# Kernel tuning notes

Measured on AMD Instinct MI355X. Metric: run time of the kernel, lower is better.

Reference implementation:

```python
import jax, jax.numpy as jnp
import numpy as np

EPS = 1e-5

def _point_batch_norm(x, gamma, beta):
    # BatchNorm1d over channel dim of (B, N, C): stats over (B, N), biased var (training mode)
    mu = jnp.mean(x, axis=(0, 1))
    var = jnp.var(x, axis=(0, 1))
    return (x - mu) * jax.lax.rsqrt(var + EPS) * gamma + beta

def setup_inputs() -> dict:
    key = jax.random.key(0)
    ks = jax.random.split(key, 10)
    B, M, N, K = 4, 16384, 32768, 16
    C, Cs, O = 64, 64, 64
    curr_coords = jax.random.normal(ks[0], (B, M, 3), jnp.float32)
    curr_feat = jax.random.normal(ks[1], (B, M, C), jnp.float32)
    skip_coords = jax.random.normal(ks[2], (B, N, 3), jnp.float32)
    skip_feat = jax.random.normal(ks[3], (B, N, Cs), jnp.float32)
    upsampling_idxs = jax.random.randint(ks[4], (B, N, K), 0, M, jnp.int64)
    s1 = 1.0 / np.sqrt(C)
    s2 = 1.0 / np.sqrt(Cs)
    W1 = jax.random.uniform(ks[5], (C, O), jnp.float32, -s1, s1)
    b1 = jax.random.uniform(ks[6], (O,), jnp.float32, -s1, s1)
    W2 = jax.random.uniform(ks[7], (Cs, O), jnp.float32, -s2, s2)
    b2 = jax.random.uniform(ks[8], (O,), jnp.float32, -s2, s2)
    g1 = jnp.ones((O,), jnp.float32); beta1 = jnp.zeros((O,), jnp.float32)
    g2 = jnp.ones((O,), jnp.float32); beta2 = jnp.zeros((O,), jnp.float32)
    return {
        "curr_coords": curr_coords, "curr_feat": curr_feat,
        "skip_coords": skip_coords, "skip_feat": skip_feat,
        "upsampling_idxs": upsampling_idxs,
        "W1": W1, "b1": b1, "g1": g1, "beta1": beta1,
        "W2": W2, "b2": b2, "g2": g2, "beta2": beta2,
    }

def reference(curr_coords, curr_feat, skip_coords, skip_feat, upsampling_idxs,
              W1, b1, g1, beta1, W2, b2, g2, beta2):
    # Gather K-NN neighbor features per skip point: (B, N, K, C), then max over K
    gathered = jax.vmap(lambda f, i: f[i])(curr_feat, upsampling_idxs)
    pooled = jnp.max(gathered, axis=2)  # (B, N, C)
    # proj: Linear -> PointBatchNorm -> ReLU
    h = jax.nn.relu(_point_batch_norm(pooled @ W1 + b1, g1, beta1))
    # proj_skip on skip features
    hs = jax.nn.relu(_point_batch_norm(skip_feat @ W2 + b2, g2, beta2))
    return jnp.concatenate([skip_coords, h, hs], axis=-1)  # (B, N, 3 + 2*O)
```

## Files before the change

kernel.cpp:

```cpp
#include <hip/hip_runtime.h>
#include <hip/hip_bf16.h>

#define BB 4
#define MM 16384
#define NN 32768
#define KK 16
#define ROWS (BB * NN)
#define OUTW 131
#define RPW 32
#define A_BLOCKS (ROWS / (RPW * 4))

__global__ __launch_bounds__(256) void k_pool_proj(
    const float* __restrict__ cf, const int* __restrict__ idxs,
    const float* __restrict__ scoord,
    const float* __restrict__ W1, const float* __restrict__ b1,
    float* __restrict__ out, float* __restrict__ acc)
{
    __shared__ float pool[4][64];
    __shared__ float lsum[64], lsq[64];
    const int lane = threadIdx.x & 63;
    const int wv   = threadIdx.x >> 6;
    if (threadIdx.x < 64) { lsum[threadIdx.x] = 0.f; lsq[threadIdx.x] = 0.f; }
    __syncthreads();

    float w[64];
#pragma unroll
    for (int c = 0; c < 64; ++c) w[c] = W1[c * 64 + lane];
    const float bias = b1[lane];

    float psum = 0.f, psq = 0.f;
    const int gw = blockIdx.x * 4 + wv;
    for (int r0 = 0; r0 < RPW; ++r0) {
        const int r = gw * RPW + r0;
        const int b = r >> 15;
        int mi = 0;
        if (lane < KK) mi = idxs[r * KK + lane];
        float pmax = -3.402823466e38f;
#pragma unroll
        for (int k = 0; k < KK; ++k) {
            const int m = __shfl(mi, k);
            pmax = fmaxf(pmax, cf[(((b << 14) + m) << 6) + lane]);
        }
        pool[wv][lane] = pmax;
        __builtin_amdgcn_wave_barrier();

        float y = bias;
#pragma unroll
        for (int c = 0; c < 64; ++c) y = fmaf(pool[wv][c], w[c], y);
        __builtin_amdgcn_wave_barrier();

        const size_t ob = (size_t)r * OUTW;
        out[ob + 3 + lane] = y;
        if (lane < 3) out[ob + lane] = scoord[r * 3 + lane];
        psum += y; psq += y * y;
    }
    atomicAdd(&lsum[lane], psum);
    atomicAdd(&lsq[lane], psq);
    __syncthreads();
    if (threadIdx.x < 64) {
        atomicAdd(&acc[threadIdx.x],      lsum[threadIdx.x]);
        atomicAdd(&acc[64 + threadIdx.x], lsq[threadIdx.x]);
    }
}

__global__ __launch_bounds__(256) void k_skip_proj(
    const float* __restrict__ sf,
    const float* __restrict__ W2, const float* __restrict__ b2,
    float* __restrict__ out, float* __restrict__ acc)
{
    __shared__ float srow[4][64];
    __shared__ float lsum[64], lsq[64];
    const int lane = threadIdx.x & 63;
    const int wv   = threadIdx.x >> 6;
    if (threadIdx.x < 64) { lsum[threadIdx.x] = 0.f; lsq[threadIdx.x] = 0.f; }
    __syncthreads();

    float w[64];
#pragma unroll
    for (int c = 0; c < 64; ++c) w[c] = W2[c * 64 + lane];
    const float bias = b2[lane];

    float psum = 0.f, psq = 0.f;
    const int gw = blockIdx.x * 4 + wv;
    for (int r0 = 0; r0 < RPW; ++r0) {
        const int r = gw * RPW + r0;
        srow[wv][lane] = sf[(size_t)r * 64 + lane];
        __builtin_amdgcn_wave_barrier();

        float y = bias;
#pragma unroll
        for (int c = 0; c < 64; ++c) y = fmaf(srow[wv][c], w[c], y);
        __builtin_amdgcn_wave_barrier();

        const size_t ob = (size_t)r * OUTW;
        out[ob + 67 + lane] = y;
        psum += y; psq += y * y;
    }
    atomicAdd(&lsum[lane], psum);
    atomicAdd(&lsq[lane], psq);
    __syncthreads();
    if (threadIdx.x < 64) {
        atomicAdd(&acc[128 + threadIdx.x], lsum[threadIdx.x]);
        atomicAdd(&acc[192 + threadIdx.x], lsq[threadIdx.x]);
    }
}

__global__ void k_stats(float* __restrict__ ws,
                        const float* __restrict__ g1, const float* __restrict__ be1,
                        const float* __restrict__ g2, const float* __restrict__ be2)
{
    const int o = threadIdx.x;
    const float inv = 1.0f / (float)ROWS;
    float m1 = ws[o] * inv;
    float v1 = ws[64 + o] * inv - m1 * m1;
    float a1 = g1[o] * rsqrtf(v1 + 1e-5f);
    ws[256 + o] = a1;
    ws[384 + o] = be1[o] - m1 * a1;
    float m2 = ws[128 + o] * inv;
    float v2 = ws[192 + o] * inv - m2 * m2;
    float a2 = g2[o] * rsqrtf(v2 + 1e-5f);
    ws[256 + 64 + o] = a2;
    ws[384 + 64 + o] = be2[o] - m2 * a2;
}

__global__ __launch_bounds__(256) void k_finalize(float* __restrict__ out,
                                                  const float* __restrict__ ws)
{
    const size_t T  = (size_t)gridDim.x * blockDim.x;
    const size_t t0 = (size_t)blockIdx.x * blockDim.x + threadIdx.x;
#pragma unroll
    for (int i = 0; i < 4; ++i) {
        const size_t e = t0 + (size_t)i * T;
        const size_t r = e >> 7;
        const int    j = (int)(e & 127);
        const size_t ad = r * OUTW + 3 + j;
        const float v = out[ad];
        out[ad] = fmaxf(fmaf(v, ws[256 + j], ws[384 + j]), 0.f);
    }
}

extern "C" void kernel_launch(void* const* d_in, const int* in_sizes, int n_in,
                              void* d_out, int out_size, void* d_ws, size_t ws_size,
                              hipStream_t stream)
{
    const float* cf     = (const float*)d_in[1];
    const float* scoord = (const float*)d_in[2];
    const float* sf     = (const float*)d_in[3];
    const int*   idxs   = (const int*)  d_in[4];
    const float* W1     = (const float*)d_in[5];
    const float* b1     = (const float*)d_in[6];
    const float* g1     = (const float*)d_in[7];
    const float* be1    = (const float*)d_in[8];
    const float* W2     = (const float*)d_in[9];
    const float* b2     = (const float*)d_in[10];
    const float* g2     = (const float*)d_in[11];
    const float* be2    = (const float*)d_in[12];
    float* out = (float*)d_out;
    float* ws  = (float*)d_ws;

    hipMemsetAsync(ws, 0, 256 * sizeof(float), stream);
    k_pool_proj<<<A_BLOCKS, 256, 0, stream>>>(cf, idxs, scoord, W1, b1, out, ws);
    k_skip_proj<<<A_BLOCKS, 256, 0, stream>>>(sf, W2, b2, out, ws);
    k_stats<<<1, 64, 0, stream>>>(ws, g1, be1, g2, be2);
    k_finalize<<<16384, 256, 0, stream>>>(out, ws);
}
```

Baseline: 290.1 us.

## Fuse batch-norm finalize into projection kernels via grid barrier, keep rows in LDS

Each projection kernel now holds its pre-norm outputs in shared memory, accumulates channel statistics, waits at a software grid-wide barrier, then applies batch norm and ReLU and writes the final output once. This drops the separate stats and finalize kernels and their full read-modify-write pass over the output. It also maps pool blocks to XCDs by batch for L2 locality, uses readlane broadcasts instead of LDS for the matvec, and prefetches indices and skip rows. The spin barrier relies on all 1024 blocks being co-resident, which risks deadlock if occupancy is lower than assumed.

```diff
diff --git a/kernel.cpp b/kernel.cpp
--- a/kernel.cpp
+++ b/kernel.cpp
@@ -1,5 +1,4 @@
 #include <hip/hip_runtime.h>
-#include <hip/hip_bf16.h>
 
 #define BB 4
 #define MM 16384
@@ -8,134 +7,171 @@
 #define ROWS (BB * NN)
 #define OUTW 131
 #define RPW 32
-#define A_BLOCKS (ROWS / (RPW * 4))
-
-__global__ __launch_bounds__(256) void k_pool_proj(
+#define GRID_A 1024
+#define GRID_B 1024
+
+
+__device__ __forceinline__ float bcast(float v, int sl) {
+    return __int_as_float(__builtin_amdgcn_readlane(__float_as_int(v), sl));
+}
+
+__device__ __forceinline__ void grid_barrier(int* bar, int nblk) {
+    __threadfence();
+    __syncthreads();
+    if (threadIdx.x == 0) {
+        __hip_atomic_fetch_add(bar, 1, __ATOMIC_ACQ_REL, __HIP_MEMORY_SCOPE_AGENT);
+        while (__hip_atomic_load(bar, __ATOMIC_ACQUIRE, __HIP_MEMORY_SCOPE_AGENT) < nblk)
+            __builtin_amdgcn_s_sleep(8);
+    }
+    __syncthreads();
+}
+
+__global__ __launch_bounds__(256, 4) void k_pool_proj(
     const float* __restrict__ cf, const int* __restrict__ idxs,
     const float* __restrict__ scoord,
     const float* __restrict__ W1, const float* __restrict__ b1,
-    float* __restrict__ out, float* __restrict__ acc)
+    const float* __restrict__ g1, const float* __restrict__ be1,
+    float* __restrict__ out, float* __restrict__ ws)
 {
-    __shared__ float pool[4][64];
+    __shared__ float ysav[4][RPW][64];
     __shared__ float lsum[64], lsq[64];
     const int lane = threadIdx.x & 63;
     const int wv   = threadIdx.x >> 6;
     if (threadIdx.x < 64) { lsum[threadIdx.x] = 0.f; lsq[threadIdx.x] = 0.f; }
     __syncthreads();
 
-    float w[64];
-#pragma unroll
-    for (int c = 0; c < 64; ++c) w[c] = W1[c * 64 + lane];
+    const int w     = blockIdx.x;
+    const int xcd   = w & 7;
+    const int batch = xcd >> 1;
+    const int lb    = (w >> 3) + ((xcd & 1) << 7);
+    const int rbase = batch * NN + (lb * 4 + wv) * RPW;
+
+    float wr[64];
+#pragma unroll
+    for (int c = 0; c < 64; ++c) wr[c] = W1[c * 64 + lane];
     const float bias = b1[lane];
+    const float* cfb = cf + ((size_t)batch * MM * 64);
 
     float psum = 0.f, psq = 0.f;
-    const int gw = blockIdx.x * 4 + wv;
-    for (int r0 = 0; r0 < RPW; ++r0) {
-        const int r = gw * RPW + r0;
-        const int b = r >> 15;
-        int mi = 0;
-        if (lane < KK) mi = idxs[r * KK + lane];
-        float pmax = -3.402823466e38f;
-#pragma unroll
-        for (int k = 0; k < KK; ++k) {
-            const int m = __shfl(mi, k);
-            pmax = fmaxf(pmax, cf[(((b << 14) + m) << 6) + lane]);
+    int mi4 = idxs[(size_t)rbase * KK + lane];
+    for (int r0 = 0; r0 < RPW; r0 += 4) {
+        int mi4n = 0;
+        if (r0 + 4 < RPW) mi4n = idxs[(size_t)(rbase + r0 + 4) * KK + lane];
+#pragma unroll
+        for (int rr = 0; rr < 4; ++rr) {
+            float p0 = -3.402823466e38f, p1 = p0;
+#pragma unroll
+            for (int k = 0; k < KK; k += 2) {
+                const int m0 = __builtin_amdgcn_readlane(mi4, (rr << 4) + k);
+                const int m1 = __builtin_amdgcn_readlane(mi4, (rr << 4) + k + 1);
+                p0 = fmaxf(p0, cfb[((size_t)m0 << 6) + lane]);
+                p1 = fmaxf(p1, cfb[((size_t)m1 << 6) + lane]);
+            }
+            const float pmax = fmaxf(p0, p1);
+            float a0 = 0.f, a1 = 0.f, a2 = 0.f, a3 = 0.f;
+#pragma unroll
+            for (int c = 0; c < 64; c += 4) {
+                a0 = fmaf(bcast(pmax, c + 0), wr[c + 0], a0);
+                a1 = fmaf(bcast(pmax, c + 1), wr[c + 1], a1);
+                a2 = fmaf(bcast(pmax, c + 2), wr[c + 2], a2);
+                a3 = fmaf(bcast(pmax, c + 3), wr[c + 3], a3);
+            }
+            const float y = bias + ((a0 + a1) + (a2 + a3));
+            ysav[wv][r0 + rr][lane] = y;
+            psum += y; psq += y * y;
+            const int r = rbase + r0 + rr;
+            if (lane < 3) out[(size_t)r * OUTW + lane] = scoord[(size_t)r * 3 + lane];
         }
-        pool[wv][lane] = pmax;
-        __builtin_amdgcn_wave_barrier();
-
-        float y = bias;
-#pragma unroll
-        for (int c = 0; c < 64; ++c) y = fmaf(pool[wv][c], w[c], y);
-        __builtin_amdgcn_wave_barrier();
-
-        const size_t ob = (size_t)r * OUTW;
-        out[ob + 3 + lane] = y;
-        if (lane < 3) out[ob + lane] = scoord[r * 3 + lane];
-        psum += y; psq += y * y;
-    }
+        mi4 = mi4n;
+    }
+
     atomicAdd(&lsum[lane], psum);
     atomicAdd(&lsq[lane], psq);
     __syncthreads();
     if (threadIdx.x < 64) {
-        atomicAdd(&acc[threadIdx.x],      lsum[threadIdx.x]);
-        atomicAdd(&acc[64 + threadIdx.x], lsq[threadIdx.x]);
-    }
-}
-
-__global__ __launch_bounds__(256) void k_skip_proj(
+        atomicAdd(&ws[threadIdx.x],      lsum[threadIdx.x]);
+        atomicAdd(&ws[64 + threadIdx.x], lsq[threadIdx.x]);
+    }
+
+    grid_barrier((int*)ws + 256, GRID_A);
+
+    const float inv = 1.0f / (float)ROWS;
+    const float s  = __hip_atomic_load(&ws[lane],      __ATOMIC_RELAXED, __HIP_MEMORY_SCOPE_AGENT);
+    const float q  = __hip_atomic_load(&ws[64 + lane], __ATOMIC_RELAXED, __HIP_MEMORY_SCOPE_AGENT);
+    const float m  = s * inv;
+    const float v  = q * inv - m * m;
+    const float a  = g1[lane] * rsqrtf(v + 1e-5f);
+    const float c0 = be1[lane] - m * a;
+    for (int r0 = 0; r0 < RPW; ++r0) {
+        const float y = ysav[wv][r0][lane];
+        out[(size_t)(rbase + r0) * OUTW + 3 + lane] = fmaxf(fmaf(y, a, c0), 0.f);
+    }
+}
+
+__global__ __launch_bounds__(256, 4) void k_skip_proj(
     const float* __restrict__ sf,
     const float* __restrict__ W2, const float* __restrict__ b2,
-    float* __restrict__ out, float* __restrict__ acc)
+    const float* __restrict__ g2, const float* __restrict__ be2,
+    float* __restrict__ out, float* __restrict__ ws)
 {
-    __shared__ float srow[4][64];
+    __shared__ float ysav[4][RPW][64];
     __shared__ float lsum[64], lsq[64];
     const int lane = threadIdx.x & 63;
     const int wv   = threadIdx.x >> 6;
     if (threadIdx.x < 64) { lsum[threadIdx.x] = 0.f; lsq[threadIdx.x] = 0.f; }
     __syncthreads();
 
-    float w[64];
-#pragma unroll
-    for (int c = 0; c < 64; ++c) w[c] = W2[c * 64 + lane];
+    const int rbase = (blockIdx.x * 4 + wv) * RPW;
+
+    float wr[64];
+#pragma unroll
+    for (int c = 0; c < 64; ++c) wr[c] = W2[c * 64 + lane];
     const float bias = b2[lane];
 
+    const float4* sf4 = (const float4*)sf;
     float psum = 0.f, psq = 0.f;
-    const int gw = blockIdx.x * 4 + wv;
-    for (int r0 = 0; r0 < RPW; ++r0) {
-        const int r = gw * RPW + r0;
-        srow[wv][lane] = sf[(size_t)r * 64 + lane];
-        __builtin_amdgcn_wave_barrier();
-
-        float y = bias;
-#pragma unroll
-        for (int c = 0; c < 64; ++c) y = fmaf(srow[wv][c], w[c], y);
-        __builtin_amdgcn_wave_barrier();
-
-        const size_t ob = (size_t)r * OUTW;
-        out[ob + 67 + lane] = y;
-        psum += y; psq += y * y;
-    }
+    float4 x4 = sf4[(size_t)rbase * 16 + lane];
+    for (int g = 0; g < RPW; g += 4) {
+        float4 x4n = make_float4(0.f, 0.f, 0.f, 0.f);
+        if (g + 4 < RPW) x4n = sf4[(size_t)(rbase + g + 4) * 16 + lane];
+#pragma unroll
+        for (int rr = 0; rr < 4; ++rr) {
+            float a0 = 0.f, a1 = 0.f, a2 = 0.f, a3 = 0.f;
+#pragma unroll
+            for (int c = 0; c < 64; c += 4) {
+                const int sl = rr * 16 + (c >> 2);
+                a0 = fmaf(bcast(x4.x, sl), wr[c + 0], a0);
+                a1 = fmaf(bcast(x4.y, sl), wr[c + 1], a1);
+                a2 = fmaf(bcast(x4.z, sl), wr[c + 2], a2);
+                a3 = fmaf(bcast(x4.w, sl), wr[c + 3], a3);
+            }
+            const float y = bias + ((a0 + a1) + (a2 + a3));
+            ysav[wv][g + rr][lane] = y;
+            psum += y; psq += y * y;
+        }
+        x4 = x4n;
+    }
+
     atomicAdd(&lsum[lane], psum);
     atomicAdd(&lsq[lane], psq);
     __syncthreads();
     if (threadIdx.x < 64) {
-        atomicAdd(&acc[128 + threadIdx.x], lsum[threadIdx.x]);
-        atomicAdd(&acc[192 + threadIdx.x], lsq[threadIdx.x]);
-    }
-}
-
-__global__ void k_stats(float* __restrict__ ws,
-                        const float* __restrict__ g1, const float* __restrict__ be1,
-                        const float* __restrict__ g2, const float* __restrict__ be2)
-{
-    const int o = threadIdx.x;
+        atomicAdd(&ws[128 + threadIdx.x], lsum[threadIdx.x]);
+        atomicAdd(&ws[192 + threadIdx.x], lsq[threadIdx.x]);
+    }
+
+    grid_barrier((int*)ws + 257, GRID_B);
+
     const float inv = 1.0f / (float)ROWS;
-    float m1 = ws[o] * inv;
-    float v1 = ws[64 + o] * inv - m1 * m1;
-    float a1 = g1[o] * rsqrtf(v1 + 1e-5f);
-    ws[256 + o] = a1;
-    ws[384 + o] = be1[o] - m1 * a1;
-    float m2 = ws[128 + o] * inv;
-    float v2 = ws[192 + o] * inv - m2 * m2;
-    float a2 = g2[o] * rsqrtf(v2 + 1e-5f);
-    ws[256 + 64 + o] = a2;
-    ws[384 + 64 + o] = be2[o] - m2 * a2;
-}
-
-__global__ __launch_bounds__(256) void k_finalize(float* __restrict__ out,
-                                                  const float* __restrict__ ws)
-{
-    const size_t T  = (size_t)gridDim.x * blockDim.x;
-    const size_t t0 = (size_t)blockIdx.x * blockDim.x + threadIdx.x;
-#pragma unroll
-    for (int i = 0; i < 4; ++i) {
-        const size_t e = t0 + (size_t)i * T;
-        const size_t r = e >> 7;
-        const int    j = (int)(e & 127);
-        const size_t ad = r * OUTW + 3 + j;
-        const float v = out[ad];
-        out[ad] = fmaxf(fmaf(v, ws[256 + j], ws[384 + j]), 0.f);
+    const float s  = __hip_atomic_load(&ws[128 + lane], __ATOMIC_RELAXED, __HIP_MEMORY_SCOPE_AGENT);
+    const float q  = __hip_atomic_load(&ws[192 + lane], __ATOMIC_RELAXED, __HIP_MEMORY_SCOPE_AGENT);
+    const float m  = s * inv;
+    const float v  = q * inv - m * m;
+    const float a  = g2[lane] * rsqrtf(v + 1e-5f);
+    const float c0 = be2[lane] - m * a;
+    for (int r0 = 0; r0 < RPW; ++r0) {
+        const float y = ysav[wv][r0][lane];
+        out[(size_t)(rbase + r0) * OUTW + 67 + lane] = fmaxf(fmaf(y, a, c0), 0.f);
     }
 }
 
@@ -158,9 +194,7 @@
     float* out = (float*)d_out;
     float* ws  = (float*)d_ws;
 
-    hipMemsetAsync(ws, 0, 256 * sizeof(float), stream);
-    k_pool_proj<<<A_BLOCKS, 256, 0, stream>>>(cf, idxs, scoord, W1, b1, out, ws);
-    k_skip_proj<<<A_BLOCKS, 256, 0, stream>>>(sf, W2, b2, out, ws);
-    k_stats<<<1, 64, 0, stream>>>(ws, g1, be1, g2, be2);
-    k_finalize<<<16384, 256, 0, stream>>>(out, ws);
-}
+    hipMemsetAsync(ws, 0, 2048, stream);
+    k_pool_proj<<<GRID_A, 256, 0, stream>>>(cf, idxs, scoord, W1, b1, g1, be1, out, ws);
+    k_skip_proj<<<GRID_B, 256, 0, stream>>>(sf, W2, b2, g2, be2, out, ws);
+}
```

New measurement: 692.7 us. 139% more time.

## Batch eight rows per wave, broadcast via readlane, remap blocks by XCD/batch

Applied to the files above, without the earlier changes.

Both projection kernels now handle eight rows at a time. Pooled or input values stay in registers and are broadcast with readlane instead of round-tripping through LDS with wave barriers. The gather kernel remaps block IDs so each pair of XCDs serves a single batch, which should keep that batch's feature table local in L2. It also splits the K-max into two independent chains to expose more memory-level parallelism. The trade-offs are higher register pressure under launch_bounds(256,4), and a mapping that hardcodes 1024 blocks and 8 XCDs.

```diff
diff --git a/kernel.cpp b/kernel.cpp
--- a/kernel.cpp
+++ b/kernel.cpp
@@ -1,5 +1,4 @@
 #include <hip/hip_runtime.h>
-#include <hip/hip_bf16.h>
 
 #define BB 4
 #define MM 16384
@@ -8,51 +7,72 @@
 #define ROWS (BB * NN)
 #define OUTW 131
 #define RPW 32
-#define A_BLOCKS (ROWS / (RPW * 4))
+#define A_BLOCKS 1024
 
-__global__ __launch_bounds__(256) void k_pool_proj(
+__device__ __forceinline__ float bcast(float v, int sl) {
+    return __int_as_float(__builtin_amdgcn_readlane(__float_as_int(v), sl));
+}
+
+__global__ __launch_bounds__(256, 4) void k_pool_proj(
     const float* __restrict__ cf, const int* __restrict__ idxs,
     const float* __restrict__ scoord,
     const float* __restrict__ W1, const float* __restrict__ b1,
     float* __restrict__ out, float* __restrict__ acc)
 {
-    __shared__ float pool[4][64];
     __shared__ float lsum[64], lsq[64];
     const int lane = threadIdx.x & 63;
     const int wv   = threadIdx.x >> 6;
     if (threadIdx.x < 64) { lsum[threadIdx.x] = 0.f; lsq[threadIdx.x] = 0.f; }
     __syncthreads();
 
-    float w[64];
+    const int w     = blockIdx.x;
+    const int xcd   = w & 7;
+    const int batch = xcd >> 1;
+    const int lb    = (w >> 3) + ((xcd & 1) << 7);
+    const int rbase = batch * NN + (lb * 4 + wv) * RPW;
+
+    float wreg[64];
 #pragma unroll
-    for (int c = 0; c < 64; ++c) w[c] = W1[c * 64 + lane];
+    for (int c = 0; c < 64; ++c) wreg[c] = W1[c * 64 + lane];
     const float bias = b1[lane];
+    const float* cfb = cf + ((size_t)batch << 20);
 
     float psum = 0.f, psq = 0.f;
-    const int gw = blockIdx.x * 4 + wv;
-    for (int r0 = 0; r0 < RPW; ++r0) {
-        const int r = gw * RPW + r0;
-        const int b = r >> 15;
-        int mi = 0;
-        if (lane < KK) mi = idxs[r * KK + lane];
-        float pmax = -3.402823466e38f;
+    for (int g = 0; g < RPW; g += 8) {
+        float pm[8];
 #pragma unroll
-        for (int k = 0; k < KK; ++k) {
-            const int m = __shfl(mi, k);
-            pmax = fmaxf(pmax, cf[(((b << 14) + m) << 6) + lane]);
+        for (int r = 0; r < 8; ++r) {
+            const int row = rbase + g + r;
+            int mi = 0;
+            if (lane < KK) mi = idxs[row * KK + lane];
+            float p0 = -3.402823466e38f, p1 = p0;
+#pragma unroll
+            for (int k = 0; k < KK; k += 2) {
+                const int m0 = __shfl(mi, k);
+                const int m1 = __shfl(mi, k + 1);
+                p0 = fmaxf(p0, cfb[((size_t)m0 << 6) + lane]);
+                p1 = fmaxf(p1, cfb[((size_t)m1 << 6) + lane]);
+            }
+            pm[r] = fmaxf(p0, p1);
         }
-        pool[wv][lane] = pmax;
-        __builtin_amdgcn_wave_barrier();
-
-        float y = bias;
+        float y[8];
 #pragma unroll
-        for (int c = 0; c < 64; ++c) y = fmaf(pool[wv][c], w[c], y);
-        __builtin_amdgcn_wave_barrier();
-
-        const size_t ob = (size_t)r * OUTW;
-        out[ob + 3 + lane] = y;
-        if (lane < 3) out[ob + lane] = scoord[r * 3 + lane];
-        psum += y; psq += y * y;
+        for (int r = 0; r < 8; ++r) y[r] = bias;
+#pragma unroll
+        for (int c = 0; c < 64; ++c) {
+            const float wc = wreg[c];
+#pragma unroll
+            for (int r = 0; r < 8; ++r)
+                y[r] = fmaf(bcast(pm[r], c), wc, y[r]);
+        }
+#pragma unroll
+        for (int r = 0; r < 8; ++r) {
+            const int row = rbase + g + r;
+            const size_t ob = (size_t)row * OUTW;
+            out[ob + 3 + lane] = y[r];
+            if (lane < 3) out[ob + lane] = scoord[row * 3 + lane];
+            psum += y[r]; psq += y[r] * y[r];
+        }
     }
     atomicAdd(&lsum[lane], psum);
     atomicAdd(&lsq[lane], psq);
@@ -63,38 +83,46 @@
     }
 }
 
-__global__ __launch_bounds__(256) void k_skip_proj(
+__global__ __launch_bounds__(256, 4) void k_skip_proj(
     const float* __restrict__ sf,
     const float* __restrict__ W2, const float* __restrict__ b2,
     float* __restrict__ out, float* __restrict__ acc)
 {
-    __shared__ float srow[4][64];
     __shared__ float lsum[64], lsq[64];
     const int lane = threadIdx.x & 63;
     const int wv   = threadIdx.x >> 6;
     if (threadIdx.x < 64) { lsum[threadIdx.x] = 0.f; lsq[threadIdx.x] = 0.f; }
     __syncthreads();
 
-    float w[64];
+    const int rbase = (blockIdx.x * 4 + wv) * RPW;
+
+    float wreg[64];
 #pragma unroll
-    for (int c = 0; c < 64; ++c) w[c] = W2[c * 64 + lane];
+    for (int c = 0; c < 64; ++c) wreg[c] = W2[c * 64 + lane];
     const float bias = b2[lane];
 
     float psum = 0.f, psq = 0.f;
-    const int gw = blockIdx.x * 4 + wv;
-    for (int r0 = 0; r0 < RPW; ++r0) {
-        const int r = gw * RPW + r0;
-        srow[wv][lane] = sf[(size_t)r * 64 + lane];
-        __builtin_amdgcn_wave_barrier();
-
-        float y = bias;
+    for (int g = 0; g < RPW; g += 8) {
+        float xm[8];
 #pragma unroll
-        for (int c = 0; c < 64; ++c) y = fmaf(srow[wv][c], w[c], y);
-        __builtin_amdgcn_wave_barrier();
-
-        const size_t ob = (size_t)r * OUTW;
-        out[ob + 67 + lane] = y;
-        psum += y; psq += y * y;
+        for (int r = 0; r < 8; ++r)
+            xm[r] = sf[(size_t)(rbase + g + r) * 64 + lane];
+        float y[8];
+#pragma unroll
+        for (int r = 0; r < 8; ++r) y[r] = bias;
+#pragma unroll
+        for (int c = 0; c < 64; ++c) {
+            const float wc = wreg[c];
+#pragma unroll
+            for (int r = 0; r < 8; ++r)
+                y[r] = fmaf(bcast(xm[r], c), wc, y[r]);
+        }
+#pragma unroll
+        for (int r = 0; r < 8; ++r) {
+            const size_t ob = (size_t)(rbase + g + r) * OUTW;
+            out[ob + 67 + lane] = y[r];
+            psum += y[r]; psq += y[r] * y[r];
+        }
     }
     atomicAdd(&lsum[lane], psum);
     atomicAdd(&lsq[lane], psq);
```

Result: slower. 816.5 us (+181.4%).

## Use fp16 MFMA for both projections and remap blocks per XCD for gather locality

Applied to the files above, without the earlier changes.

Replaces the per-lane scalar FMA projection loops with 16x16x32 fp16 MFMA tiles in both projection kernels. Pooled and skip rows are staged as fp16 in padded LDS, and the gather now reads four rows' indices per wave load with dual max accumulators. Blocks are remapped so each pair of XCDs works on one batch, so the gathered curr_feat slices stay in a smaller set of L2 caches. The fp16 conversion of activations and weights lowers precision before BatchNorm, which may cost accuracy.

```diff
diff --git a/kernel.cpp b/kernel.cpp
--- a/kernel.cpp
+++ b/kernel.cpp
@@ -1,5 +1,4 @@
 #include <hip/hip_runtime.h>
-#include <hip/hip_bf16.h>
 
 #define BB 4
 #define MM 16384
@@ -7,8 +6,37 @@
 #define KK 16
 #define ROWS (BB * NN)
 #define OUTW 131
-#define RPW 32
-#define A_BLOCKS (ROWS / (RPW * 4))
+#define TPW 2
+#define RPWAVE (TPW * 16)
+#define A_BLOCKS (ROWS / (RPWAVE * 4))
+#define APAD 72
+
+
+typedef _Float16 half8 __attribute__((ext_vector_type(8)));
+typedef float f32x4 __attribute__((ext_vector_type(4)));
+
+__device__ __forceinline__ half8 load_bfrag(const float* __restrict__ W, int lane, int ot, int kt) {
+    const int kb  = kt * 32 + ((lane >> 4) << 3);
+    const int col = ot * 16 + (lane & 15);
+    half8 b;
+#pragma unroll
+    for (int j = 0; j < 8; ++j) b[j] = (_Float16)W[(kb + j) * 64 + col];
+    return b;
+}
+
+__device__ __forceinline__ float gmax16(const float* __restrict__ cfb, int mi, int base, int lane) {
+    float a0 = -3.402823466e38f, a1 = a0;
+#pragma unroll
+    for (int k = 0; k < KK; k += 2) {
+        const int m0 = __builtin_amdgcn_readlane(mi, base + k);
+        const int m1 = __builtin_amdgcn_readlane(mi, base + k + 1);
+        a0 = fmaxf(a0, cfb[((size_t)m0 << 6) + lane]);
+        a1 = fmaxf(a1, cfb[((size_t)m1 << 6) + lane]);
+    }
+    return fmaxf(a0, a1);
+}
+
+#define MFMA16(a, b, c) __builtin_amdgcn_mfma_f32_16x16x32_f16(a, b, c, 0, 0, 0)
 
 __global__ __launch_bounds__(256) void k_pool_proj(
     const float* __restrict__ cf, const int* __restrict__ idxs,
@@ -16,46 +44,88 @@
     const float* __restrict__ W1, const float* __restrict__ b1,
     float* __restrict__ out, float* __restrict__ acc)
 {
-    __shared__ float pool[4][64];
+    __shared__ _Float16 ah[4][16][APAD];
     __shared__ float lsum[64], lsq[64];
     const int lane = threadIdx.x & 63;
     const int wv   = threadIdx.x >> 6;
     if (threadIdx.x < 64) { lsum[threadIdx.x] = 0.f; lsq[threadIdx.x] = 0.f; }
     __syncthreads();
 
-    float w[64];
-#pragma unroll
-    for (int c = 0; c < 64; ++c) w[c] = W1[c * 64 + lane];
-    const float bias = b1[lane];
-
-    float psum = 0.f, psq = 0.f;
-    const int gw = blockIdx.x * 4 + wv;
-    for (int r0 = 0; r0 < RPW; ++r0) {
-        const int r = gw * RPW + r0;
-        const int b = r >> 15;
-        int mi = 0;
-        if (lane < KK) mi = idxs[r * KK + lane];
-        float pmax = -3.402823466e38f;
-#pragma unroll
-        for (int k = 0; k < KK; ++k) {
-            const int m = __shfl(mi, k);
-            pmax = fmaxf(pmax, cf[(((b << 14) + m) << 6) + lane]);
-        }
-        pool[wv][lane] = pmax;
-        __builtin_amdgcn_wave_barrier();
-
-        float y = bias;
-#pragma unroll
-        for (int c = 0; c < 64; ++c) y = fmaf(pool[wv][c], w[c], y);
-        __builtin_amdgcn_wave_barrier();
-
-        const size_t ob = (size_t)r * OUTW;
-        out[ob + 3 + lane] = y;
-        if (lane < 3) out[ob + lane] = scoord[r * 3 + lane];
-        psum += y; psq += y * y;
-    }
-    atomicAdd(&lsum[lane], psum);
-    atomicAdd(&lsq[lane], psq);
+    const int w     = blockIdx.x;
+    const int xcd   = w & 7;
+    const int batch = xcd >> 1;
+    const int lb    = (w >> 3) + ((xcd & 1) << 7);
+    const int rbase = batch * NN + (lb * 4 + wv) * RPWAVE;
+    const float* cfb = cf + ((size_t)batch << 20);
+
+    const half8 b00 = load_bfrag(W1, lane, 0, 0), b01 = load_bfrag(W1, lane, 0, 1);
+    const half8 b10 = load_bfrag(W1, lane, 1, 0), b11 = load_bfrag(W1, lane, 1, 1);
+    const half8 b20 = load_bfrag(W1, lane, 2, 0), b21 = load_bfrag(W1, lane, 2, 1);
+    const half8 b30 = load_bfrag(W1, lane, 3, 0), b31 = load_bfrag(W1, lane, 3, 1);
+    const float bias0 = b1[(lane & 15) +  0], bias1 = b1[(lane & 15) + 16];
+    const float bias2 = b1[(lane & 15) + 32], bias3 = b1[(lane & 15) + 48];
+
+    float ps0 = 0.f, ps1 = 0.f, ps2 = 0.f, ps3 = 0.f;
+    float pq0 = 0.f, pq1 = 0.f, pq2 = 0.f, pq3 = 0.f;
+
+#pragma unroll
+    for (int t = 0; t < TPW; ++t) {
+        const int tb = rbase + t * 16;
+#pragma unroll
+        for (int s = 0; s < 4; ++s) {
+            const int r4 = tb + s * 4;
+            const int mi = idxs[(size_t)r4 * KK + lane];
+            const float p0 = gmax16(cfb, mi,  0, lane);
+            const float p1 = gmax16(cfb, mi, 16, lane);
+            const float p2 = gmax16(cfb, mi, 32, lane);
+            const float p3 = gmax16(cfb, mi, 48, lane);
+            ah[wv][s * 4 + 0][lane] = (_Float16)p0;
+            ah[wv][s * 4 + 1][lane] = (_Float16)p1;
+            ah[wv][s * 4 + 2][lane] = (_Float16)p2;
+            ah[wv][s * 4 + 3][lane] = (_Float16)p3;
+            if (lane < 3) {
+                out[(size_t)(r4 + 0) * OUTW + lane] = scoord[(size_t)(r4 + 0) * 3 + lane];
+                out[(size_t)(r4 + 1) * OUTW + lane] = scoord[(size_t)(r4 + 1) * 3 + lane];
+                out[(size_t)(r4 + 2) * OUTW + lane] = scoord[(size_t)(r4 + 2) * 3 + lane];
+                out[(size_t)(r4 + 3) * OUTW + lane] = scoord[(size_t)(r4 + 3) * 3 + lane];
+            }
+        }
+        __builtin_amdgcn_wave_barrier();
+
+        const half8 a0 = *(const half8*)&ah[wv][lane & 15][((lane >> 4) << 3)];
+        const half8 a1 = *(const half8*)&ah[wv][lane & 15][32 + ((lane >> 4) << 3)];
+
+        f32x4 ac0 = {0.f, 0.f, 0.f, 0.f}, ac1 = ac0, ac2 = ac0, ac3 = ac0;
+        ac0 = MFMA16(a0, b00, ac0); ac0 = MFMA16(a1, b01, ac0);
+        ac1 = MFMA16(a0, b10, ac1); ac1 = MFMA16(a1, b11, ac1);
+        ac2 = MFMA16(a0, b20, ac2); ac2 = MFMA16(a1, b21, ac2);
+        ac3 = MFMA16(a0, b30, ac3); ac3 = MFMA16(a1, b31, ac3);
+        __builtin_amdgcn_wave_barrier();
+
+        const int rl = tb + ((lane >> 4) << 2);
+        const int cl = lane & 15;
+#pragma unroll
+        for (int j = 0; j < 4; ++j) {
+            const size_t ob = (size_t)(rl + j) * OUTW + 3 + cl;
+            const float y0 = ac0[j] + bias0;
+            const float y1 = ac1[j] + bias1;
+            const float y2 = ac2[j] + bias2;
+            const float y3 = ac3[j] + bias3;
+            out[ob +  0] = y0;
+            out[ob + 16] = y1;
+            out[ob + 32] = y2;
+            out[ob + 48] = y3;
+            ps0 += y0; pq0 += y0 * y0;
+            ps1 += y1; pq1 += y1 * y1;
+            ps2 += y2; pq2 += y2 * y2;
+            ps3 += y3; pq3 += y3 * y3;
+        }
+    }
+
+    atomicAdd(&lsum[(lane & 15) +  0], ps0); atomicAdd(&lsq[(lane & 15) +  0], pq0);
+    atomicAdd(&lsum[(lane & 15) + 16], ps1); atomicAdd(&lsq[(lane & 15) + 16], pq1);
+    atomicAdd(&lsum[(lane & 15) + 32], ps2); atomicAdd(&lsq[(lane & 15) + 32], pq2);
+    atomicAdd(&lsum[(lane & 15) + 48], ps3); atomicAdd(&lsq[(lane & 15) + 48], pq3);
     __syncthreads();
     if (threadIdx.x < 64) {
         atomicAdd(&acc[threadIdx.x],      lsum[threadIdx.x]);
@@ -68,36 +138,76 @@
     const float* __restrict__ W2, const float* __restrict__ b2,
     float* __restrict__ out, float* __restrict__ acc)
 {
-    __shared__ float srow[4][64];
+    __shared__ _Float16 ah[4][16][APAD];
     __shared__ float lsum[64], lsq[64];
     const int lane = threadIdx.x & 63;
     const int wv   = threadIdx.x >> 6;
     if (threadIdx.x < 64) { lsum[threadIdx.x] = 0.f; lsq[threadIdx.x] = 0.f; }
     __syncthreads();
 
-    float w[64];
-#pragma unroll
-    for (int c = 0; c < 64; ++c) w[c] = W2[c * 64 + lane];
-    const float bias = b2[lane];
-
-    float psum = 0.f, psq = 0.f;
-    const int gw = blockIdx.x * 4 + wv;
-    for (int r0 = 0; r0 < RPW; ++r0) {
-        const int r = gw * RPW + r0;
-        srow[wv][lane] = sf[(size_t)r * 64 + lane];
-        __builtin_amdgcn_wave_barrier();
-
-        float y = bias;
-#pragma unroll
-        for (int c = 0; c < 64; ++c) y = fmaf(srow[wv][c], w[c], y);
-        __builtin_amdgcn_wave_barrier();
-
-        const size_t ob = (size_t)r * OUTW;
-        out[ob + 67 + lane] = y;
-        psum += y; psq += y * y;
-    }
-    atomicAdd(&lsum[lane], psum);
-    atomicAdd(&lsq[lane], psq);
+    const int rbase = (blockIdx.x * 4 + wv) * RPWAVE;
+
+    const half8 b00 = load_bfrag(W2, lane, 0, 0), b01 = load_bfrag(W2, lane, 0, 1);
+    const half8 b10 = load_bfrag(W2, lane, 1, 0), b11 = load_bfrag(W2, lane, 1, 1);
+    const half8 b20 = load_bfrag(W2, lane, 2, 0), b21 = load_bfrag(W2, lane, 2, 1);
+    const half8 b30 = load_bfrag(W2, lane, 3, 0), b31 = load_bfrag(W2, lane, 3, 1);
+    const float bias0 = b2[(lane & 15) +  0], bias1 = b2[(lane & 15) + 16];
+    const float bias2 = b2[(lane & 15) + 32], bias3 = b2[(lane & 15) + 48];
+
+    float ps0 = 0.f, ps1 = 0.f, ps2 = 0.f, ps3 = 0.f;
+    float pq0 = 0.f, pq1 = 0.f, pq2 = 0.f, pq3 = 0.f;
+
+#pragma unroll
+    for (int t = 0; t < TPW; ++t) {
+        const int tb = rbase + t * 16;
+#pragma unroll
+        for (int s = 0; s < 4; ++s) {
+            const int r4 = tb + s * 4;
+            const float x0 = sf[(size_t)(r4 + 0) * 64 + lane];
+            const float x1 = sf[(size_t)(r4 + 1) * 64 + lane];
+            const float x2 = sf[(size_t)(r4 + 2) * 64 + lane];
+            const float x3 = sf[(size_t)(r4 + 3) * 64 + lane];
+            ah[wv][s * 4 + 0][lane] = (_Float16)x0;
+            ah[wv][s * 4 + 1][lane] = (_Float16)x1;
+            ah[wv][s * 4 + 2][lane] = (_Float16)x2;
+            ah[wv][s * 4 + 3][lane] = (_Float16)x3;
+        }
+        __builtin_amdgcn_wave_barrier();
+
+        const half8 a0 = *(const half8*)&ah[wv][lane & 15][((lane >> 4) << 3)];
+        const half8 a1 = *(const half8*)&ah[wv][lane & 15][32 + ((lane >> 4) << 3)];
+
+        f32x4 ac0 = {0.f, 0.f, 0.f, 0.f}, ac1 = ac0, ac2 = ac0, ac3 = ac0;
+        ac0 = MFMA16(a0, b00, ac0); ac0 = MFMA16(a1, b01, ac0);
+        ac1 = MFMA16(a0, b10, ac1); ac1 = MFMA16(a1, b11, ac1);
+        ac2 = MFMA16(a0, b20, ac2); ac2 = MFMA16(a1, b21, ac2);
+        ac3 = MFMA16(a0, b30, ac3); ac3 = MFMA16(a1, b31, ac3);
+        __builtin_amdgcn_wave_barrier();
+
+        const int rl = tb + ((lane >> 4) << 2);
+        const int cl = lane & 15;
+#pragma unroll
+        for (int j = 0; j < 4; ++j) {
+            const size_t ob = (size_t)(rl + j) * OUTW + 67 + cl;
+            const float y0 = ac0[j] + bias0;
+            const float y1 = ac1[j] + bias1;
+            const float y2 = ac2[j] + bias2;
+            const float y3 = ac3[j] + bias3;
+            out[ob +  0] = y0;
+            out[ob + 16] = y1;
+            out[ob + 32] = y2;
+            out[ob + 48] = y3;
+            ps0 += y0; pq0 += y0 * y0;
+            ps1 += y1; pq1 += y1 * y1;
+            ps2 += y2; pq2 += y2 * y2;
+            ps3 += y3; pq3 += y3 * y3;
+        }
+    }
+
+    atomicAdd(&lsum[(lane & 15) +  0], ps0); atomicAdd(&lsq[(lane & 15) +  0], pq0);
+    atomicAdd(&lsum[(lane & 15) + 16], ps1); atomicAdd(&lsq[(lane & 15) + 16], pq1);
+    atomicAdd(&lsum[(lane & 15) + 32], ps2); atomicAdd(&lsq[(lane & 15) + 32], pq2);
+    atomicAdd(&lsum[(lane & 15) + 48], ps3); atomicAdd(&lsq[(lane & 15) + 48], pq3);
     __syncthreads();
     if (threadIdx.x < 64) {
         atomicAdd(&acc[128 + threadIdx.x], lsum[threadIdx.x]);
```

Result: slower. 317.9 us (+9.6%).
